# Performance work log

Hardware: AMD Instinct MI355X
Metric: run time of the kernel (lower is better)

The kernel has to match this reference:

```python
import jax, jax.numpy as jnp
import numpy as np


def setup_inputs() -> dict:
    key = jax.random.key(0)
    bs, n_heads, ch, length = 4, 8, 64, 2048
    width = 3 * n_heads * ch  # 1536
    qkv = jax.random.normal(key, (bs, width, length), dtype=jnp.float32)
    return {"qkv": qkv, "n_heads": n_heads}


def reference(qkv, n_heads):
    bs, width, length = qkv.shape
    ch = width // (3 * n_heads)
    # reshape to (bs*heads, 3*ch, length) then split into q, k, v of (B, ch, L)
    qkv_r = qkv.reshape(bs * n_heads, 3 * ch, length)
    q, k, v = qkv_r[:, :ch], qkv_r[:, ch:2 * ch], qkv_r[:, 2 * ch:]
    scale = ch ** (-0.5)
    # weight = bmm(q^T, k) * scale -> (B, L_q, L_k)
    weight = jnp.einsum('bct,bcs->bts', q, k) * scale
    weight = jax.nn.softmax(weight.astype(jnp.float32), axis=-1).astype(qkv.dtype)
    # a = bmm(v, weight^T) -> (B, ch, L)
    a = jnp.einsum('bcs,bts->bct', v, weight)
    return a.reshape(bs, n_heads * ch, length)
```

## Files before the change

### kernel.cpp

```cpp
#include <hip/hip_runtime.h>

typedef __bf16 bf16;
typedef __attribute__((ext_vector_type(8)))  __bf16 bf16x8;
typedef __attribute__((ext_vector_type(16))) float  f32x16;

#define LEN   2048
#define CH    64
#define HEADS 32

union PackU { unsigned u[4]; bf16x8 v; };

static __device__ inline unsigned pack2(float lo, float hi) {
  union { bf16 h[2]; unsigned u; } p;
  p.h[0] = (bf16)lo; p.h[1] = (bf16)hi;
  return p.u;
}

__global__ __launch_bounds__(256) void prep_kernel(const float* __restrict__ qkv,
                                                   bf16* __restrict__ ws) {
  __shared__ float tile[64][65];
  const int tIdx = blockIdx.x;
  const int g    = blockIdx.y;
  const int tid  = threadIdx.x;
  const int s0   = tIdx * 64;
  const float* K = qkv + (g * 192 + 64)  * LEN;
  const float* V = qkv + (g * 192 + 128) * LEN;

  {
    const int c0 = tid >> 6, s = tid & 63;
#pragma unroll
    for (int i = 0; i < 16; ++i) {
      const int c = c0 + i * 4;
      tile[c][s] = K[c * LEN + s0 + s];
    }
  }
  __syncthreads();

  bf16* dst = ws + ((size_t)g * 32 + tIdx) * 8192;
#pragma unroll
  for (int it = 0; it < 2; ++it) {
    const int c2 = tid + it * 256;
    const int r  = c2 >> 6, ln = c2 & 63;
    const int nn = ln & 31, hh = ln >> 5;
    const int kb = r >> 1,  mb = r & 1;
    const int s  = mb * 32 + nn;
    const int cg = kb * 2 + hh;
    bf16x8 o;
#pragma unroll
    for (int j = 0; j < 8; ++j) o[j] = (bf16)tile[cg * 8 + j][s];
    *(bf16x8*)(dst + c2 * 8) = o;
  }
#pragma unroll
  for (int it = 0; it < 2; ++it) {
    const int c2  = tid + it * 256;
    const int r   = c2 >> 6, ln = c2 & 63;
    const int nn  = ln & 31, hh = ln >> 5;
    const int kbs = r >> 1,  mbo = r & 1;
    const int k8  = kbs * 2 + hh;
    const int pa  = 32 * (k8 >> 2) + 8 * ((k8 >> 1) & 1) + 4 * (k8 & 1);
    const float* src = V + (mbo * 32 + nn) * LEN + s0 + pa;
    const float4 a = *(const float4*)src;
    const float4 b = *(const float4*)(src + 16);
    bf16x8 o;
    o[0] = (bf16)a.x; o[1] = (bf16)a.y; o[2] = (bf16)a.z; o[3] = (bf16)a.w;
    o[4] = (bf16)b.x; o[5] = (bf16)b.y; o[6] = (bf16)b.z; o[7] = (bf16)b.w;
    *(bf16x8*)(dst + 4096 + c2 * 8) = o;
  }
}

__global__ __launch_bounds__(256, 2) void attn_kernel(const float* __restrict__ qkv,
                                                      const bf16* __restrict__ ws,
                                                      float* __restrict__ out) {
  const int tid  = threadIdx.x;
  const int lane = tid & 63;
  const int wv   = tid >> 6;
  const int n    = lane & 31;
  const int h    = lane >> 5;
  const int g    = blockIdx.x & 31;
  const int jb   = blockIdx.x >> 5;
  const int t0   = jb * 128 + wv * 32;

  const bf16* wsg = ws + (size_t)g * (32 * 8192);

  const float qs = 0.125f * 1.44269504088896340736f;
  const float* Q = qkv + g * (192 * LEN);
  bf16x8 qf[4];
#pragma unroll
  for (int kb = 0; kb < 4; ++kb)
#pragma unroll
    for (int jj = 0; jj < 8; ++jj)
      qf[kb][jj] = (bf16)(Q[(kb * 16 + h * 8 + jj) * LEN + t0 + n] * qs);

  f32x16 o_acc[2];
#pragma unroll
  for (int mb = 0; mb < 2; ++mb)
#pragma unroll
    for (int r = 0; r < 16; ++r) o_acc[mb][r] = 0.f;
  float l_acc = 0.f;

  f32x16 zf;
#pragma unroll
  for (int r = 0; r < 16; ++r) zf[r] = 0.f;

  for (int i = 0; i < 32; ++i) {
    const bf16* tb = wsg + i * 8192;

    bf16x8 ka[8], vf[8];
#pragma unroll
    for (int r = 0; r < 8; ++r)
      ka[r] = *(const bf16x8*)(tb + r * 512 + lane * 8);
#pragma unroll
    for (int r = 0; r < 8; ++r)
      vf[r] = *(const bf16x8*)(tb + 4096 + r * 512 + lane * 8);

    f32x16 sf[2];
    __builtin_amdgcn_s_setprio(1);
#pragma unroll
    for (int mb = 0; mb < 2; ++mb)
      sf[mb] = __builtin_amdgcn_mfma_f32_32x32x16_bf16(ka[mb], qf[0], zf, 0, 0, 0);
#pragma unroll
    for (int kb = 1; kb < 4; ++kb)
#pragma unroll
      for (int mb = 0; mb < 2; ++mb)
        sf[mb] = __builtin_amdgcn_mfma_f32_32x32x16_bf16(ka[kb * 2 + mb], qf[kb], sf[mb], 0, 0, 0);
    __builtin_amdgcn_s_setprio(0);

    PackU frag[4];
    float ls = 0.f;
#pragma unroll
    for (int mb = 0; mb < 2; ++mb)
#pragma unroll
      for (int u = 0; u < 4; ++u) {
        const float p0 = __builtin_amdgcn_exp2f(sf[mb][4 * u + 0]);
        const float p1 = __builtin_amdgcn_exp2f(sf[mb][4 * u + 1]);
        const float p2 = __builtin_amdgcn_exp2f(sf[mb][4 * u + 2]);
        const float p3 = __builtin_amdgcn_exp2f(sf[mb][4 * u + 3]);
        ls += (p0 + p1) + (p2 + p3);
        const int kb   = 2 * mb + (u & 1);
        const int base = 2 * (u >> 1);
        frag[kb].u[base]     = pack2(p0, p1);
        frag[kb].u[base + 1] = pack2(p2, p3);
      }
    l_acc += ls;

    __builtin_amdgcn_s_setprio(1);
#pragma unroll
    for (int kbs = 0; kbs < 4; ++kbs)
#pragma unroll
      for (int mbo = 0; mbo < 2; ++mbo)
        o_acc[mbo] = __builtin_amdgcn_mfma_f32_32x32x16_bf16(vf[kbs * 2 + mbo], frag[kbs].v, o_acc[mbo], 0, 0, 0);
    __builtin_amdgcn_s_setprio(0);
  }

  const float lt  = l_acc + __shfl_xor(l_acc, 32);
  const float inv = 1.0f / lt;
  float* og = out + g * (CH * LEN);
#pragma unroll
  for (int mbo = 0; mbo < 2; ++mbo)
#pragma unroll
    for (int r = 0; r < 16; ++r) {
      const int c = 32 * mbo + (r & 3) + 8 * (r >> 2) + 4 * h;
      og[c * LEN + t0 + n] = o_acc[mbo][r] * inv;
    }
}

extern "C" void kernel_launch(void* const* d_in, const int* in_sizes, int n_in,
                              void* d_out, int out_size, void* d_ws, size_t ws_size,
                              hipStream_t stream) {
  const float* qkv = (const float*)d_in[0];
  float* out = (float*)d_out;
  bf16* ws = (bf16*)d_ws;

  prep_kernel<<<dim3(32, HEADS), 256, 0, stream>>>(qkv, ws);
  attn_kernel<<<dim3(512), 256, 0, stream>>>(qkv, ws, out);
}
```

Measured before the change: 131.2 us.

## Split key loop across two wave groups per block and reduce via LDS

Doubles block size so two groups of four waves each process alternating key/value tiles for the same query rows, then combines partial outputs and softmax denominators through shared memory before writing. This is meant to raise the number of resident waves per CU and shorten each wave's serial loop, improving latency hiding. It adds an LDS reduction with two barriers and tighter launch bounds that could force register spills.

```diff
diff --git a/kernel.cpp b/kernel.cpp
--- a/kernel.cpp
+++ b/kernel.cpp
@@ -68,12 +68,16 @@
   }
 }
 
-__global__ __launch_bounds__(256, 2) void attn_kernel(const float* __restrict__ qkv,
+__global__ __launch_bounds__(512, 4) void attn_kernel(const float* __restrict__ qkv,
                                                       const bf16* __restrict__ ws,
                                                       float* __restrict__ out) {
+  __shared__ __align__(16) float fx[9344];
+
   const int tid  = threadIdx.x;
   const int lane = tid & 63;
-  const int wv   = tid >> 6;
+  const int w    = tid >> 6;
+  const int wv   = w & 3;
+  const int sg   = w >> 2;
   const int n    = lane & 31;
   const int h    = lane >> 5;
   const int g    = blockIdx.x & 31;
@@ -102,7 +106,8 @@
 #pragma unroll
   for (int r = 0; r < 16; ++r) zf[r] = 0.f;
 
-  for (int i = 0; i < 32; ++i) {
+  for (int it = 0; it < 16; ++it) {
+    const int i = 2 * it + sg;
     const bf16* tb = wsg + i * 8192;
 
     bf16x8 ka[8], vf[8];
@@ -152,16 +157,41 @@
     __builtin_amdgcn_s_setprio(0);
   }
 
-  const float lt  = l_acc + __shfl_xor(l_acc, 32);
-  const float inv = 1.0f / lt;
-  float* og = out + g * (CH * LEN);
-#pragma unroll
-  for (int mbo = 0; mbo < 2; ++mbo)
-#pragma unroll
-    for (int r = 0; r < 16; ++r) {
-      const int c = 32 * mbo + (r & 3) + 8 * (r >> 2) + 4 * h;
-      og[c * LEN + t0 + n] = o_acc[mbo][r] * inv;
-    }
+  float lt = l_acc + __shfl_xor(l_acc, 32);
+  float* lx = fx + 9216;
+
+  __syncthreads();
+  if (sg == 1) {
+#pragma unroll
+    for (int mbo = 0; mbo < 2; ++mbo)
+#pragma unroll
+      for (int u = 0; u < 4; ++u) {
+        float4 st;
+        st.x = o_acc[mbo][4 * u + 0];
+        st.y = o_acc[mbo][4 * u + 1];
+        st.z = o_acc[mbo][4 * u + 2];
+        st.w = o_acc[mbo][4 * u + 3];
+        *(float4*)&fx[wv * 2304 + lane * 36 + mbo * 16 + 4 * u] = st;
+      }
+    if (h == 0) lx[wv * 32 + n] = lt;
+  }
+  __syncthreads();
+  if (sg == 0) {
+    const float inv = 1.0f / (lt + lx[wv * 32 + n]);
+    float* og = out + g * (CH * LEN);
+#pragma unroll
+    for (int mbo = 0; mbo < 2; ++mbo)
+#pragma unroll
+      for (int u = 0; u < 4; ++u) {
+        const float4 q = *(const float4*)&fx[wv * 2304 + lane * 36 + mbo * 16 + 4 * u];
+#pragma unroll
+        for (int j = 0; j < 4; ++j) {
+          const int r = 4 * u + j;
+          const int c = 32 * mbo + (r & 3) + 8 * (r >> 2) + 4 * h;
+          og[c * LEN + t0 + n] = (o_acc[mbo][r] + ((const float*)&q)[j]) * inv;
+        }
+      }
+  }
 }
 
 extern "C" void kernel_launch(void* const* d_in, const int* in_sizes, int n_in,
@@ -172,5 +202,5 @@
   bf16* ws = (bf16*)d_ws;
 
   prep_kernel<<<dim3(32, HEADS), 256, 0, stream>>>(qkv, ws);
-  attn_kernel<<<dim3(512), 256, 0, stream>>>(qkv, ws, out);
-}
+  attn_kernel<<<dim3(512), 512, 0, stream>>>(qkv, ws, out);
+}
```

After: 166.6 us. 27.0% more time.
